# Performance work log

Measured on AMD Instinct MI355X. Metric: run time of the kernel, lower is better.

## Reference

```python
import jax, jax.numpy as jnp
import numpy as np

EPS = 1e-12  # torch F.normalize clamp
D = 4        # max_displacement


def _l2norm_c(x):
    # L2 normalize over channel dim (axis=1), matching F.normalize(p=2, dim=1)
    n = jnp.sqrt(jnp.sum(x * x, axis=1, keepdims=True))
    return x / jnp.maximum(n, EPS)


def setup_inputs() -> dict:
    key = jax.random.key(0)
    k1, k2 = jax.random.split(key)
    B, C, H, W = 4, 128, 128, 256
    feat1 = jax.random.normal(k1, (B, C, H, W), dtype=jnp.float32)
    feat2_warped = jax.random.normal(k2, (B, C, H, W), dtype=jnp.float32)
    return {"feat1": feat1, "feat2_warped": feat2_warped}


def reference(feat1, feat2_warped):
    B, C, H, W = feat1.shape
    f1 = _l2norm_c(feat1)
    f2 = _l2norm_c(feat2_warped)
    # zero-pad spatial dims by D (matches F.unfold padding=D)
    f2p = jnp.pad(f2, ((0, 0), (0, 0), (D, D), (D, D)))
    costs = []
    # fixed (2D+1)^2 = 81 displacements, row-major (dy, dx) to match unfold ordering
    for dy in range(2 * D + 1):
        for dx in range(2 * D + 1):
            shifted = jax.lax.slice(f2p, (0, 0, dy, dx), (B, C, dy + H, dx + W))
            costs.append(jnp.sum(f1 * shifted, axis=1) / C)  # (B,H,W)
    cost = jnp.stack(costs, axis=1)  # (B, 81, H, W)
    return jax.nn.leaky_relu(cost, negative_slope=0.1)
```

## Files before the change

### kernel.cpp

```cpp
#include <hip/hip_runtime.h>

#define B_ 4
#define C_ 128
#define H_ 128
#define W_ 256
#define HW_ (H_ * W_)
#define ND 81
#define TH 8
#define TW 16
#define HR 16
#define WCOL 32
#define KC 32
#define NCHUNK (C_ / KC)
#define NTHREADS 512

typedef short bf16x8 __attribute__((ext_vector_type(8)));
typedef float f32x4 __attribute__((ext_vector_type(4)));
typedef float f32x4v __attribute__((ext_vector_type(4)));
typedef unsigned int u32x4 __attribute__((ext_vector_type(4)));

__device__ __forceinline__ int swz(int px, int byteInHalf) {
    int r = px >> 1;
    int base = (r << 7) + ((px & 1) << 6) + byteInHalf;
    return base ^ ((r & 7) << 4);
}

__device__ __forceinline__ unsigned int pack_bf16(float a, float b) {
    unsigned int ua = __float_as_uint(a);
    unsigned int ub = __float_as_uint(b);
    ua = (ua + 0x7FFFu + ((ua >> 16) & 1u)) >> 16;
    ub = (ub + 0x7FFFu + ((ub >> 16) & 1u)) >> 16;
    return (ub << 16) | (ua & 0xFFFFu);
}

__device__ __forceinline__ void accum_sq(unsigned int u, float& ss) {
    float lo = __uint_as_float(u << 16);
    float hi = __uint_as_float(u & 0xFFFF0000u);
    ss += lo * lo + hi * hi;
}

__global__ __launch_bounds__(NTHREADS)
void corr81_kernel(const float* __restrict__ f1g, const float* __restrict__ f2g,
                   float* __restrict__ out) {
    __shared__ __align__(16) unsigned short f2s[HR * WCOL * KC];
    __shared__ __align__(16) unsigned short f1s[TH * TW * KC];
    __shared__ float invn2[HR * WCOL];
    __shared__ float invn1[TH * TW];

    const int tid  = threadIdx.x;
    const int lane = tid & 63;
    const int wave = tid >> 6;
    const int col  = lane & 15;
    const int quad = lane >> 4;

    const int flat = blockIdx.x + 16 * blockIdx.y + 256 * blockIdx.z;
    const int orig = (flat & 7) * 128 + (flat >> 3);
    const int w0 = (orig & 15) * TW;
    const int h0 = ((orig >> 4) & 15) * TH;
    const int b  = orig >> 8;
    const size_t inBase = (size_t)b * C_ * HW_;

    const int g2  = tid & 7;
    const int cp2 = (tid >> 3) & 15;
    const int rq  = tid >> 7;
    const int gw2 = w0 - 4 + g2 * 4;
    const bool colok2 = (gw2 >= 0) && (gw2 < W_);

    const int g1  = tid & 3;
    const int cp1 = (tid >> 2) & 15;
    const int r1  = tid >> 6;
    const float* src1 = f1g + inBase + (size_t)(h0 + r1) * W_ + (w0 + g1 * 4);

    const int aOff = swz(wave * 16 + col, quad * 16);

    f32x4 acc[9][2];
#pragma unroll
    for (int d = 0; d < 9; ++d) {
        acc[d][0] = (f32x4)0.f;
        acc[d][1] = (f32x4)0.f;
    }

    char* f2sW = (char*)f2s;
    char* f1sW = (char*)f1s;
    const char* f2sR = (const char*)f2s;
    const char* f1sR = (const char*)f1s;

    float ss2 = 0.f, ss1 = 0.f;

    f32x4v A0[4], A1[4], B0, B1;

#pragma unroll
    for (int i = 0; i < 4; ++i) {
        int r  = i * 4 + rq;
        int gh = h0 - 4 + r;
        if (colok2 && gh >= 0 && gh < H_) {
            const float* s = f2g + inBase + (size_t)(cp2 * 2) * HW_ + (size_t)gh * W_ + gw2;
            A0[i] = *(const f32x4v*)s;
            A1[i] = *(const f32x4v*)(s + HW_);
        } else {
            A0[i] = (f32x4v)0.f;
            A1[i] = (f32x4v)0.f;
        }
    }
    {
        const float* s = src1 + (size_t)(cp1 * 2) * HW_;
        B0 = *(const f32x4v*)s;
        B1 = *(const f32x4v*)(s + HW_);
    }

    for (int ch = 0; ch < NCHUNK; ++ch) {
#pragma unroll
        for (int i = 0; i < 4; ++i) {
            int r = i * 4 + rq;
#pragma unroll
            for (int j = 0; j < 4; ++j) {
                int px = r * 32 + g2 * 4 + j;
                *(unsigned int*)(f2sW + swz(px, cp2 * 4)) = pack_bf16(A0[i][j], A1[i][j]);
            }
        }
        if (ch < NCHUNK - 1) {
            const int kc0 = (ch + 1) * KC;
#pragma unroll
            for (int i = 0; i < 4; ++i) {
                int r  = i * 4 + rq;
                int gh = h0 - 4 + r;
                if (colok2 && gh >= 0 && gh < H_) {
                    const float* s = f2g + inBase + (size_t)(kc0 + cp2 * 2) * HW_ + (size_t)gh * W_ + gw2;
                    A0[i] = *(const f32x4v*)s;
                    A1[i] = *(const f32x4v*)(s + HW_);
                } else {
                    A0[i] = (f32x4v)0.f;
                    A1[i] = (f32x4v)0.f;
                }
            }
        }
#pragma unroll
        for (int j = 0; j < 4; ++j) {
            int px = r1 * 16 + g1 * 4 + j;
            *(unsigned int*)(f1sW + swz(px, cp1 * 4)) = pack_bf16(B0[j], B1[j]);
        }
        if (ch < NCHUNK - 1) {
            const float* s = src1 + (size_t)((ch + 1) * KC + cp1 * 2) * HW_;
            B0 = *(const f32x4v*)s;
            B1 = *(const f32x4v*)(s + HW_);
        }

        __syncthreads();

#pragma unroll
        for (int j = 0; j < 4; ++j) {
            u32x4 v = *(const u32x4*)(f2sR + swz(tid, j * 16));
            accum_sq(v[0], ss2); accum_sq(v[1], ss2);
            accum_sq(v[2], ss2); accum_sq(v[3], ss2);
        }
        {
            u32x4 v = *(const u32x4*)(f1sR + swz(tid >> 2, (tid & 3) * 16));
            accum_sq(v[0], ss1); accum_sq(v[1], ss1);
            accum_sq(v[2], ss1); accum_sq(v[3], ss1);
        }
        if (ch == NCHUNK - 1) {
            invn2[tid] = 1.f / fmaxf(sqrtf(ss2), 1e-12f);
            float t1 = ss1 + __shfl_xor(ss1, 1);
            t1 += __shfl_xor(t1, 2);
            if ((tid & 3) == 0) invn1[tid >> 2] = 1.f / fmaxf(sqrtf(t1), 1e-12f);
        }

        __builtin_amdgcn_s_setprio(1);
        bf16x8 af = *(const bf16x8*)(f1sR + aOff);
#pragma unroll
        for (int dy = 0; dy < 9; ++dy) {
            int pb = (wave + dy) * WCOL + col;
            bf16x8 b0 = *(const bf16x8*)(f2sR + swz(pb, quad * 16));
            bf16x8 b1 = *(const bf16x8*)(f2sR + swz(pb + 16, quad * 16));
            acc[dy][0] = __builtin_amdgcn_mfma_f32_16x16x32_bf16(af, b0, acc[dy][0], 0, 0, 0);
            acc[dy][1] = __builtin_amdgcn_mfma_f32_16x16x32_bf16(af, b1, acc[dy][1], 0, 0, 0);
        }
        __builtin_amdgcn_s_setprio(0);
        __syncthreads();
    }

    const int hOut = h0 + wave;
    float* outB = out + (size_t)b * ND * HW_ + (size_t)hOut * W_;
    const float scale = 1.f / (float)C_;

#pragma unroll
    for (int dy = 0; dy < 9; ++dy) {
        int hr = wave + dy;
#pragma unroll
        for (int t = 0; t < 2; ++t) {
            float i2 = invn2[hr * WCOL + t * 16 + col];
#pragma unroll
            for (int r = 0; r < 4; ++r) {
                int row = quad * 4 + r;
                int dx = t * 16 + col - row;
                if (dx >= 0 && dx <= 8) {
                    float v = acc[dy][t][r] * invn1[wave * 16 + row] * i2 * scale;
                    v = (v >= 0.f) ? v : 0.1f * v;
                    outB[(size_t)(dy * 9 + dx) * HW_ + (w0 + row)] = v;
                }
            }
        }
    }
}

extern "C" void kernel_launch(void* const* d_in, const int* in_sizes, int n_in,
                              void* d_out, int out_size, void* d_ws, size_t ws_size,
                              hipStream_t stream) {
    const float* f1 = (const float*)d_in[0];
    const float* f2 = (const float*)d_in[1];
    float* out = (float*)d_out;
    dim3 grid(W_ / TW, H_ / TH, B_);
    corr81_kernel<<<grid, NTHREADS, 0, stream>>>(f1, f2, out);
}
```

Before: 72.92 us.

## Double-buffer LDS chunks, halve barriers, use hardware bf16 pack conversion

The single LDS staging buffer becomes two ping-pong buffers, so the next chunk is packed into the alternate buffer while the current one feeds the MFMAs. This removes one of the two barriers per chunk and prefetches two chunks ahead. Software round-to-nearest-even bf16 packing is replaced with the v_cvt_pk_bf16_f32 instruction. The norm arrays now alias buffer 0 to keep LDS usage down, which doubles staging LDS and may lower occupancy.

```diff
diff --git a/kernel.cpp b/kernel.cpp
--- a/kernel.cpp
+++ b/kernel.cpp
@@ -25,12 +25,10 @@
     return base ^ ((r & 7) << 4);
 }
 
-__device__ __forceinline__ unsigned int pack_bf16(float a, float b) {
-    unsigned int ua = __float_as_uint(a);
-    unsigned int ub = __float_as_uint(b);
-    ua = (ua + 0x7FFFu + ((ua >> 16) & 1u)) >> 16;
-    ub = (ub + 0x7FFFu + ((ub >> 16) & 1u)) >> 16;
-    return (ub << 16) | (ua & 0xFFFFu);
+__device__ __forceinline__ unsigned int cvt_pk_bf16(float a, float b) {
+    unsigned int r;
+    asm("v_cvt_pk_bf16_f32 %0, %1, %2" : "=v"(r) : "v"(a), "v"(b));
+    return r;
 }
 
 __device__ __forceinline__ void accum_sq(unsigned int u, float& ss) {
@@ -42,10 +40,10 @@
 __global__ __launch_bounds__(NTHREADS)
 void corr81_kernel(const float* __restrict__ f1g, const float* __restrict__ f2g,
                    float* __restrict__ out) {
-    __shared__ __align__(16) unsigned short f2s[HR * WCOL * KC];
-    __shared__ __align__(16) unsigned short f1s[TH * TW * KC];
-    __shared__ float invn2[HR * WCOL];
-    __shared__ float invn1[TH * TW];
+    __shared__ __align__(16) unsigned short f2s[2][HR * WCOL * KC];
+    __shared__ __align__(16) unsigned short f1s[2][TH * TW * KC];
+    float* invn2 = (float*)&f2s[0][0];
+    float* invn1 = (float*)&f1s[0][0];
 
     const int tid  = threadIdx.x;
     const int lane = tid & 63;
@@ -80,102 +78,102 @@
         acc[d][1] = (f32x4)0.f;
     }
 
-    char* f2sW = (char*)f2s;
-    char* f1sW = (char*)f1s;
-    const char* f2sR = (const char*)f2s;
-    const char* f1sR = (const char*)f1s;
-
     float ss2 = 0.f, ss1 = 0.f;
-
     f32x4v A0[4], A1[4], B0, B1;
 
-#pragma unroll
-    for (int i = 0; i < 4; ++i) {
-        int r  = i * 4 + rq;
-        int gh = h0 - 4 + r;
-        if (colok2 && gh >= 0 && gh < H_) {
-            const float* s = f2g + inBase + (size_t)(cp2 * 2) * HW_ + (size_t)gh * W_ + gw2;
-            A0[i] = *(const f32x4v*)s;
-            A1[i] = *(const f32x4v*)(s + HW_);
-        } else {
-            A0[i] = (f32x4v)0.f;
-            A1[i] = (f32x4v)0.f;
-        }
-    }
-    {
-        const float* s = src1 + (size_t)(cp1 * 2) * HW_;
-        B0 = *(const f32x4v*)s;
-        B1 = *(const f32x4v*)(s + HW_);
-    }
-
-    for (int ch = 0; ch < NCHUNK; ++ch) {
-#pragma unroll
-        for (int i = 0; i < 4; ++i) {
-            int r = i * 4 + rq;
-#pragma unroll
-            for (int j = 0; j < 4; ++j) {
-                int px = r * 32 + g2 * 4 + j;
-                *(unsigned int*)(f2sW + swz(px, cp2 * 4)) = pack_bf16(A0[i][j], A1[i][j]);
-            }
-        }
-        if (ch < NCHUNK - 1) {
-            const int kc0 = (ch + 1) * KC;
-#pragma unroll
-            for (int i = 0; i < 4; ++i) {
-                int r  = i * 4 + rq;
-                int gh = h0 - 4 + r;
-                if (colok2 && gh >= 0 && gh < H_) {
-                    const float* s = f2g + inBase + (size_t)(kc0 + cp2 * 2) * HW_ + (size_t)gh * W_ + gw2;
-                    A0[i] = *(const f32x4v*)s;
-                    A1[i] = *(const f32x4v*)(s + HW_);
-                } else {
-                    A0[i] = (f32x4v)0.f;
-                    A1[i] = (f32x4v)0.f;
-                }
-            }
-        }
-#pragma unroll
-        for (int j = 0; j < 4; ++j) {
-            int px = r1 * 16 + g1 * 4 + j;
-            *(unsigned int*)(f1sW + swz(px, cp1 * 4)) = pack_bf16(B0[j], B1[j]);
-        }
-        if (ch < NCHUNK - 1) {
-            const float* s = src1 + (size_t)((ch + 1) * KC + cp1 * 2) * HW_;
-            B0 = *(const f32x4v*)s;
-            B1 = *(const f32x4v*)(s + HW_);
-        }
-
-        __syncthreads();
-
-#pragma unroll
-        for (int j = 0; j < 4; ++j) {
-            u32x4 v = *(const u32x4*)(f2sR + swz(tid, j * 16));
-            accum_sq(v[0], ss2); accum_sq(v[1], ss2);
-            accum_sq(v[2], ss2); accum_sq(v[3], ss2);
-        }
-        {
-            u32x4 v = *(const u32x4*)(f1sR + swz(tid >> 2, (tid & 3) * 16));
-            accum_sq(v[0], ss1); accum_sq(v[1], ss1);
-            accum_sq(v[2], ss1); accum_sq(v[3], ss1);
-        }
-        if (ch == NCHUNK - 1) {
+#define ISSUE_LOADS(kc0)                                                        \
+    {                                                                           \
+        _Pragma("unroll")                                                       \
+        for (int i = 0; i < 4; ++i) {                                           \
+            int r  = i * 4 + rq;                                                \
+            int gh = h0 - 4 + r;                                                \
+            if (colok2 && gh >= 0 && gh < H_) {                                 \
+                const float* s = f2g + inBase + (size_t)((kc0) + cp2 * 2) * HW_ \
+                                 + (size_t)gh * W_ + gw2;                       \
+                A0[i] = *(const f32x4v*)s;                                      \
+                A1[i] = *(const f32x4v*)(s + HW_);                              \
+            } else {                                                            \
+                A0[i] = (f32x4v)0.f;                                            \
+                A1[i] = (f32x4v)0.f;                                            \
+            }                                                                   \
+        }                                                                       \
+        const float* s = src1 + (size_t)((kc0) + cp1 * 2) * HW_;                \
+        B0 = *(const f32x4v*)s;                                                 \
+        B1 = *(const f32x4v*)(s + HW_);                                         \
+    }
+
+#define PACK_WRITE(buf)                                                         \
+    {                                                                           \
+        char* w2 = (char*)&f2s[(buf)][0];                                       \
+        char* w1 = (char*)&f1s[(buf)][0];                                       \
+        _Pragma("unroll")                                                       \
+        for (int i = 0; i < 4; ++i) {                                           \
+            int r = i * 4 + rq;                                                 \
+            _Pragma("unroll")                                                   \
+            for (int j = 0; j < 4; ++j) {                                       \
+                int px = r * 32 + g2 * 4 + j;                                   \
+                *(unsigned int*)(w2 + swz(px, cp2 * 4)) =                       \
+                    cvt_pk_bf16(A0[i][j], A1[i][j]);                            \
+            }                                                                   \
+        }                                                                       \
+        _Pragma("unroll")                                                       \
+        for (int j = 0; j < 4; ++j) {                                           \
+            int px = r1 * 16 + g1 * 4 + j;                                      \
+            *(unsigned int*)(w1 + swz(px, cp1 * 4)) = cvt_pk_bf16(B0[j], B1[j]);\
+        }                                                                       \
+    }
+
+#define MFMA_PHASE(buf)                                                         \
+    {                                                                           \
+        const char* r2 = (const char*)&f2s[(buf)][0];                           \
+        const char* r1p = (const char*)&f1s[(buf)][0];                          \
+        __builtin_amdgcn_s_setprio(1);                                          \
+        bf16x8 af = *(const bf16x8*)(r1p + aOff);                               \
+        _Pragma("unroll")                                                       \
+        for (int dy = 0; dy < 9; ++dy) {                                        \
+            int pb = (wave + dy) * WCOL + col;                                  \
+            bf16x8 b0 = *(const bf16x8*)(r2 + swz(pb, quad * 16));              \
+            bf16x8 b1 = *(const bf16x8*)(r2 + swz(pb + 16, quad * 16));         \
+            acc[dy][0] = __builtin_amdgcn_mfma_f32_16x16x32_bf16(af, b0, acc[dy][0], 0, 0, 0); \
+            acc[dy][1] = __builtin_amdgcn_mfma_f32_16x16x32_bf16(af, b1, acc[dy][1], 0, 0, 0); \
+        }                                                                       \
+        __builtin_amdgcn_s_setprio(0);                                          \
+    }
+
+#define NORM_PHASE(buf)                                                         \
+    {                                                                           \
+        const char* r2 = (const char*)&f2s[(buf)][0];                           \
+        const char* r1p = (const char*)&f1s[(buf)][0];                          \
+        _Pragma("unroll")                                                       \
+        for (int j = 0; j < 4; ++j) {                                           \
+            u32x4 v = *(const u32x4*)(r2 + swz(tid, j * 16));                   \
+            accum_sq(v[0], ss2); accum_sq(v[1], ss2);                           \
+            accum_sq(v[2], ss2); accum_sq(v[3], ss2);                           \
+        }                                                                       \
+        u32x4 v = *(const u32x4*)(r1p + swz(tid >> 2, (tid & 3) * 16));         \
+        accum_sq(v[0], ss1); accum_sq(v[1], ss1);                               \
+        accum_sq(v[2], ss1); accum_sq(v[3], ss1);                               \
+    }
+
+    ISSUE_LOADS(0);
+    PACK_WRITE(0);
+    ISSUE_LOADS(KC);
+    __syncthreads();
+
+#pragma unroll
+    for (int k = 0; k < NCHUNK; ++k) {
+        const int bk = k & 1;
+        MFMA_PHASE(bk);
+        NORM_PHASE(bk);
+        if (k == NCHUNK - 1) {
             invn2[tid] = 1.f / fmaxf(sqrtf(ss2), 1e-12f);
             float t1 = ss1 + __shfl_xor(ss1, 1);
             t1 += __shfl_xor(t1, 2);
             if ((tid & 3) == 0) invn1[tid >> 2] = 1.f / fmaxf(sqrtf(t1), 1e-12f);
+        } else {
+            PACK_WRITE(bk ^ 1);
+            if (k < NCHUNK - 2) ISSUE_LOADS((k + 2) * KC);
         }
-
-        __builtin_amdgcn_s_setprio(1);
-        bf16x8 af = *(const bf16x8*)(f1sR + aOff);
-#pragma unroll
-        for (int dy = 0; dy < 9; ++dy) {
-            int pb = (wave + dy) * WCOL + col;
-            bf16x8 b0 = *(const bf16x8*)(f2sR + swz(pb, quad * 16));
-            bf16x8 b1 = *(const bf16x8*)(f2sR + swz(pb + 16, quad * 16));
-            acc[dy][0] = __builtin_amdgcn_mfma_f32_16x16x32_bf16(af, b0, acc[dy][0], 0, 0, 0);
-            acc[dy][1] = __builtin_amdgcn_mfma_f32_16x16x32_bf16(af, b1, acc[dy][1], 0, 0, 0);
-        }
-        __builtin_amdgcn_s_setprio(0);
         __syncthreads();
     }
 
@@ -201,6 +199,10 @@
             }
         }
     }
+#undef ISSUE_LOADS
+#undef PACK_WRITE
+#undef MFMA_PHASE
+#undef NORM_PHASE
 }
 
 extern "C" void kernel_launch(void* const* d_in, const int* in_sizes, int n_in,
```

Measured after the change: 65.45 us. -10.2%, faster.
